# Kernel optimization log

Measured on AMD Instinct MI355X. Metric: run time of the kernel, lower is better.

Reference implementation:

```python
import jax, jax.numpy as jnp
import numpy as np

NUM_HEADS = 16

def setup_inputs() -> dict:
    key = jax.random.key(0)
    ks = jax.random.split(key, 8)
    B, S, X, D = 2, 2048, 1, 1024
    scale = 1.0 / np.sqrt(D)
    return {
        "query": jax.random.normal(ks[0], (B, S, X, D), jnp.float32),
        "key": jax.random.normal(ks[1], (B, S, X, D), jnp.float32),
        "value": jax.random.normal(ks[2], (B, S, X, D), jnp.float32),
        "Wq": jax.random.normal(ks[3], (D, D), jnp.float32) * scale,
        "bq": jnp.zeros((D,), jnp.float32),
        "Wk": jax.random.normal(ks[4], (D, D), jnp.float32) * scale,
        "bk": jnp.zeros((D,), jnp.float32),
        "Wv": jax.random.normal(ks[5], (D, D), jnp.float32) * scale,
        "bv": jnp.zeros((D,), jnp.float32),
        "Wo": jax.random.normal(ks[6], (D, D), jnp.float32) * scale,
        "bo": jnp.zeros((D,), jnp.float32),
    }

def _split_heads(x, B, H):
    # [B, S, X, D] -> [B, H, S*X, depth]
    D = x.shape[-1]
    return x.reshape(B, -1, H, D // H).transpose(0, 2, 1, 3)

def reference(query, key, value, Wq, bq, Wk, bk, Wv, bv, Wo, bo):
    B, S, X, D = query.shape
    H = NUM_HEADS
    q = _split_heads(query @ Wq + bq, B, H)   # [B,H,L,dh], L=S*X
    k = _split_heads(key @ Wk + bk, B, H)
    v = _split_heads(value @ Wv + bv, B, H)
    dh = k.shape[-1]
    logits = jnp.einsum("bhqd,bhkd->bhqk", q, k) / jnp.sqrt(jnp.float32(dh))
    attn = jax.nn.softmax(logits, axis=-1)
    out = jnp.einsum("bhqk,bhkd->bhqd", attn, v)   # [B,H,L,dh]
    out = out.transpose(0, 2, 1, 3).reshape(B, S, -1, D)  # [B,S,X,D]
    return out @ Wo + bo
```

## Files before the change

### kernel.cpp

```cpp
#include <hip/hip_runtime.h>
#include <cstdint>
#include <cstddef>

typedef __bf16 bf16x8 __attribute__((ext_vector_type(8)));
typedef float f32x4 __attribute__((ext_vector_type(4)));
typedef float f32x16 __attribute__((ext_vector_type(16)));
typedef unsigned short u16;
typedef unsigned int u32;

static constexpr int Bn = 2;
static constexpr int L  = 2048;
static constexpr int Dm = 1024;
static constexpr int H  = 16;
static constexpr int DH = 64;
static constexpr int M  = Bn * L;

#define SC 0.18033688f

__device__ __forceinline__ u16 f2bf(float f) {
    union { float f; u32 u; } v; v.f = f;
    u32 u = v.u + 0x7FFFu + ((v.u >> 16) & 1u);
    return (u16)(u >> 16);
}

__device__ __forceinline__ void gl2lds16(const void* g, void* l) {
    __builtin_amdgcn_global_load_lds(
        (const __attribute__((address_space(1))) u32*)(uintptr_t)g,
        (__attribute__((address_space(3))) u32*)(uintptr_t)l, 16, 0, 0);
}

__global__ __launch_bounds__(256) void convert_in(
    const float* __restrict__ q, const float* __restrict__ k, const float* __restrict__ v,
    u16* __restrict__ dst)
{
    const float* src = (blockIdx.y == 0) ? q : (blockIdx.y == 1) ? k : v;
    u16* d = dst + (size_t)blockIdx.y * M * Dm;
    const size_t t = (size_t)blockIdx.x * 256 + threadIdx.x;
    const float4* s4 = reinterpret_cast<const float4*>(src) + t * 2;
    float4 f0 = s4[0], f1 = s4[1];
    u16 o[8] = { f2bf(f0.x), f2bf(f0.y), f2bf(f0.z), f2bf(f0.w),
                 f2bf(f1.x), f2bf(f1.y), f2bf(f1.z), f2bf(f1.w) };
    reinterpret_cast<uint4*>(d)[t] = *reinterpret_cast<uint4*>(o);
}

__global__ __launch_bounds__(256) void convert_wt(
    const float* __restrict__ Wq, const float* __restrict__ Wk,
    const float* __restrict__ Wv, const float* __restrict__ Wo,
    u16* __restrict__ dst)
{
    __shared__ u16 Ts[64][72];
    const int z = blockIdx.z;
    const float* W = (z == 0) ? Wq : (z == 1) ? Wk : (z == 2) ? Wv : Wo;
    u16* o = dst + (size_t)z * Dm * Dm;
    const int n0 = blockIdx.x * 64, k0 = blockIdx.y * 64;
    const int tid = threadIdx.x;

    {
        const int kr = tid >> 2, nc = (tid & 3) * 16;
        const float* s = W + (size_t)(k0 + kr) * Dm + n0 + nc;
        const float4* s4 = reinterpret_cast<const float4*>(s);
        float4 a = s4[0], b = s4[1], c = s4[2], d = s4[3];
        u16 t[16] = { f2bf(a.x), f2bf(a.y), f2bf(a.z), f2bf(a.w),
                      f2bf(b.x), f2bf(b.y), f2bf(b.z), f2bf(b.w),
                      f2bf(c.x), f2bf(c.y), f2bf(c.z), f2bf(c.w),
                      f2bf(d.x), f2bf(d.y), f2bf(d.z), f2bf(d.w) };
        *reinterpret_cast<uint4*>(&Ts[kr][nc])     = reinterpret_cast<uint4*>(t)[0];
        *reinterpret_cast<uint4*>(&Ts[kr][nc + 8]) = reinterpret_cast<uint4*>(t)[1];
    }
    __syncthreads();
    {
        const int nr = tid >> 2, kc = (tid & 3) * 16;
        u16 w[16];
        #pragma unroll
        for (int j = 0; j < 16; ++j) w[j] = Ts[kc + j][nr];
        u16* dptr = o + (size_t)(n0 + nr) * Dm + k0 + kc;
        *reinterpret_cast<uint4*>(dptr)     = reinterpret_cast<uint4*>(w)[0];
        *reinterpret_cast<uint4*>(dptr + 8) = reinterpret_cast<uint4*>(w)[1];
    }
}

__global__ __launch_bounds__(256) void gemm_qkv(
    const u16* __restrict__ Abuf, const u16* __restrict__ Wtb,
    const float* __restrict__ bq, const float* __restrict__ bk, const float* __restrict__ bv,
    u16* __restrict__ Qh, u16* __restrict__ Kh, u16* __restrict__ Vh)
{
    __shared__ u16 As[128 * 32];
    __shared__ u16 Bs[128 * 32];
    const int tid = threadIdx.x;
    const int wave = tid >> 6, lane = tid & 63;
    const int quad = lane >> 4, l16 = lane & 15;
    const int wr = wave >> 1, wc = wave & 1;
    const int z = blockIdx.z;
    const u16* A  = Abuf + (size_t)z * M * Dm;
    const u16* Bt = Wtb  + (size_t)z * Dm * Dm;
    const float* bias = (z == 0) ? bq : (z == 1) ? bk : bv;
    u16* out = (z == 0) ? Qh : (z == 1) ? Kh : Vh;
    const int n0 = blockIdx.x * 128, m0 = blockIdx.y * 128;

    const int srow = lane >> 2;
    const int skc  = (lane & 3) * 8;

    f32x4 acc[4][4] = {};

    for (int k0 = 0; k0 < Dm; k0 += 32) {
        __syncthreads();
        #pragma unroll
        for (int i = 0; i < 2; ++i) {
            const int ra = i * 64 + wave * 16;
            gl2lds16(A  + (size_t)(m0 + ra + srow) * Dm + k0 + skc, &As[ra * 32]);
            gl2lds16(Bt + (size_t)(n0 + ra + srow) * Dm + k0 + skc, &Bs[ra * 32]);
        }
        __syncthreads();
        bf16x8 af[4], bf[4];
        #pragma unroll
        for (int t = 0; t < 4; ++t) {
            af[t] = *reinterpret_cast<const bf16x8*>(&As[(wr * 64 + t * 16 + l16) * 32 + quad * 8]);
            bf[t] = *reinterpret_cast<const bf16x8*>(&Bs[(wc * 64 + t * 16 + l16) * 32 + quad * 8]);
        }
        #pragma unroll
        for (int mt = 0; mt < 4; ++mt)
            #pragma unroll
            for (int nt = 0; nt < 4; ++nt)
                acc[mt][nt] = __builtin_amdgcn_mfma_f32_16x16x32_bf16(af[mt], bf[nt], acc[mt][nt], 0, 0, 0);
    }

    const float qscale = (z == 0) ? SC : 1.0f;
    #pragma unroll
    for (int nt = 0; nt < 4; ++nt) {
        const int n = n0 + wc * 64 + nt * 16 + l16;
        const float badd = bias[n];
        const int h = n >> 6, d = n & 63;
        #pragma unroll
        for (int mt = 0; mt < 4; ++mt) {
            #pragma unroll
            for (int r = 0; r < 4; ++r) {
                const int m = m0 + wr * 64 + mt * 16 + quad * 4 + r;
                const int bb = m >> 11, ll = m & 2047;
                out[(((size_t)(bb * H + h)) * L + ll) * DH + d] = f2bf((acc[mt][nt][r] + badd) * qscale);
            }
        }
    }
}

__global__ __launch_bounds__(256) void transpose_v(
    const u16* __restrict__ Vh, u16* __restrict__ Vth)
{
    __shared__ u16 Ts[64][72];
    const int kt = blockIdx.x, h = blockIdx.y, b = blockIdx.z;
    const int tid = threadIdx.x;
    const size_t hb = ((size_t)(b * H + h)) * L * DH;

    {
        const int kr = tid >> 2, dc = (tid & 3) * 16;
        const u16* s = Vh + hb + (size_t)(kt * 64 + kr) * DH + dc;
        *reinterpret_cast<uint4*>(&Ts[kr][dc])     = *reinterpret_cast<const uint4*>(s);
        *reinterpret_cast<uint4*>(&Ts[kr][dc + 8]) = *reinterpret_cast<const uint4*>(s + 8);
    }
    __syncthreads();
    {
        const int dr = tid >> 2, kc = (tid & 3) * 16;
        u16 w[16];
        #pragma unroll
        for (int j = 0; j < 16; ++j) w[j] = Ts[kc + j][dr];
        u16* dptr = Vth + hb + (size_t)dr * L + kt * 64 + kc;
        *reinterpret_cast<uint4*>(dptr)     = reinterpret_cast<uint4*>(w)[0];
        *reinterpret_cast<uint4*>(dptr + 8) = reinterpret_cast<uint4*>(w)[1];
    }
}

__global__ __launch_bounds__(256) void attn(
    const u16* __restrict__ Qh, const u16* __restrict__ Kh,
    const u16* __restrict__ Vth, u16* __restrict__ ctx)
{
    __shared__ u16 KV[2 * 64 * 64];
    __shared__ u16 Os[64 * 72];

    const int tid  = threadIdx.x;
    const int wave = tid >> 6, lane = tid & 63;
    const int l31  = lane & 31, hh = lane >> 5;
    const int qt = blockIdx.x, h = blockIdx.y, b = blockIdx.z;
    const size_t hb = ((size_t)(b * H + h)) * L * DH;

    const int q0 = qt * 128 + wave * 32;

    bf16x8 qf[4];
    {
        const u16* qp = Qh + hb + (size_t)(q0 + l31) * DH + hh * 8;
        #pragma unroll
        for (int c = 0; c < 4; ++c)
            qf[c] = *reinterpret_cast<const bf16x8*>(qp + c * 16);
    }

    const int r_off = lane >> 3;
    const int s_sl  = lane & 7;

    int vbK[2], vbV[2];
    #pragma unroll
    for (int t = 0; t < 2; ++t) {
        const int rr = t * 32 + l31;
        vbK[t] = rr * 128 + ((rr & 7) << 4);
        vbV[t] = 2 * 64 * 64 + rr * 128 + ((rr & 7) << 4);
    }
    const char* ldsb = (const char*)KV;

    float rsum = 0.f;
    f32x16 oacc[2] = {};

    for (int kt = 0; kt < L / 64; ++kt) {
        __syncthreads();
        #pragma unroll
        for (int i = 0; i < 2; ++i) {
            const int rr = wave * 16 + i * 8 + r_off;
            gl2lds16(Kh  + hb + (size_t)(kt * 64 + rr) * DH + ((s_sl ^ (rr & 7)) << 3),
                     (char*)KV + (wave * 16 + i * 8) * 128);
            gl2lds16(Vth + hb + (size_t)rr * L + kt * 64 + ((s_sl ^ (rr & 7)) << 3),
                     (char*)KV + 8192 + (wave * 16 + i * 8) * 128);
        }
        __syncthreads();

        f32x16 st[2] = {};
        #pragma unroll
        for (int t = 0; t < 2; ++t) {
            #pragma unroll
            for (int c = 0; c < 4; ++c) {
                bf16x8 kf = *reinterpret_cast<const bf16x8*>(ldsb + (vbK[t] ^ (((c << 1) | hh) << 4)));
                st[t] = __builtin_amdgcn_mfma_f32_32x32x16_bf16(kf, qf[c], st[t], 0, 0, 0);
            }
        }

        bf16x8 pfrag[4];
        #pragma unroll
        for (int t = 0; t < 2; ++t) {
            float p[16];
            #pragma unroll
            for (int r = 0; r < 16; ++r) {
                p[r] = __builtin_amdgcn_exp2f(st[t][r]);
                rsum += p[r];
            }
            #pragma unroll
            for (int g = 0; g < 2; ++g) {
                float* pg = p + g * 8;
                #pragma unroll
                for (int j = 0; j < 4; ++j) {
                    asm volatile("v_permlane32_swap_b32 %0, %1" : "+v"(pg[j]), "+v"(pg[j + 4]));
                }
                u16 pk[8];
                #pragma unroll
                for (int j = 0; j < 8; ++j) pk[j] = f2bf(pg[j]);
                pfrag[t * 2 + g] = *reinterpret_cast<bf16x8*>(pk);
            }
        }

        #pragma unroll
        for (int t = 0; t < 2; ++t) {
            #pragma unroll
            for (int c = 0; c < 4; ++c) {
                bf16x8 vf = *reinterpret_cast<const bf16x8*>(ldsb + (vbV[t] ^ (((c << 1) | hh) << 4)));
                oacc[t] = __builtin_amdgcn_mfma_f32_32x32x16_bf16(vf, pfrag[c], oacc[t], 0, 0, 0);
            }
        }
    }

    rsum += __shfl_xor(rsum, 32);
    const float inv = 1.0f / rsum;

    for (int pass = 0; pass < 2; ++pass) {
        __syncthreads();
        if ((wave >> 1) == pass) {
            const int qloc = (wave & 1) * 32 + l31;
            #pragma unroll
            for (int t = 0; t < 2; ++t)
                #pragma unroll
                for (int r = 0; r < 16; ++r) {
                    const int d = t * 32 + (r & 3) + ((r >> 2) << 3) + hh * 4;
                    Os[qloc * 72 + d] = f2bf(oacc[t][r] * inv);
                }
        }
        __syncthreads();
        {
            const int row = tid >> 2, cc = (tid & 3) * 16;
            u16* dst = ctx + ((size_t)(b * L + qt * 128 + pass * 64 + row)) * Dm + h * 64 + cc;
            *reinterpret_cast<uint4*>(dst)     = *reinterpret_cast<const uint4*>(&Os[row * 72 + cc]);
            *reinterpret_cast<uint4*>(dst + 8) = *reinterpret_cast<const uint4*>(&Os[row * 72 + cc + 8]);
        }
    }
}

__global__ __launch_bounds__(256) void gemm_out(
    const u16* __restrict__ A, const u16* __restrict__ Bt,
    const float* __restrict__ bias, float* __restrict__ out)
{
    __shared__ u16 As[128 * 32];
    __shared__ u16 Bs[64 * 32];
    const int tid = threadIdx.x;
    const int wave = tid >> 6, lane = tid & 63;
    const int quad = lane >> 4, l16 = lane & 15;
    const int n0 = blockIdx.x * 64, m0 = blockIdx.y * 128;

    const int srow = lane >> 2;
    const int skc  = (lane & 3) * 8;

    f32x4 acc[2][4] = {};

    for (int k0 = 0; k0 < Dm; k0 += 32) {
        __syncthreads();
        #pragma unroll
        for (int i = 0; i < 2; ++i) {
            const int ra = i * 64 + wave * 16;
            gl2lds16(A + (size_t)(m0 + ra + srow) * Dm + k0 + skc, &As[ra * 32]);
        }
        gl2lds16(Bt + (size_t)(n0 + wave * 16 + srow) * Dm + k0 + skc, &Bs[wave * 16 * 32]);
        __syncthreads();
        bf16x8 af[2], bf[4];
        #pragma unroll
        for (int t = 0; t < 2; ++t)
            af[t] = *reinterpret_cast<const bf16x8*>(&As[(wave * 32 + t * 16 + l16) * 32 + quad * 8]);
        #pragma unroll
        for (int t = 0; t < 4; ++t)
            bf[t] = *reinterpret_cast<const bf16x8*>(&Bs[(t * 16 + l16) * 32 + quad * 8]);
        #pragma unroll
        for (int mt = 0; mt < 2; ++mt)
            #pragma unroll
            for (int nt = 0; nt < 4; ++nt)
                acc[mt][nt] = __builtin_amdgcn_mfma_f32_16x16x32_bf16(af[mt], bf[nt], acc[mt][nt], 0, 0, 0);
    }

    #pragma unroll
    for (int nt = 0; nt < 4; ++nt) {
        const int n = n0 + nt * 16 + l16;
        const float badd = bias[n];
        #pragma unroll
        for (int mt = 0; mt < 2; ++mt) {
            #pragma unroll
            for (int r = 0; r < 4; ++r) {
                const int m = m0 + wave * 32 + mt * 16 + quad * 4 + r;
                out[(size_t)m * Dm + n] = acc[mt][nt][r] + badd;
            }
        }
    }
}

extern "C" void kernel_launch(void* const* d_in, const int* in_sizes, int n_in,
                              void* d_out, int out_size, void* d_ws, size_t ws_size,
                              hipStream_t stream) {
    const float* q  = (const float*)d_in[0];
    const float* k  = (const float*)d_in[1];
    const float* v  = (const float*)d_in[2];
    const float* Wq = (const float*)d_in[3];
    const float* bq = (const float*)d_in[4];
    const float* Wk = (const float*)d_in[5];
    const float* bk = (const float*)d_in[6];
    const float* Wv = (const float*)d_in[7];
    const float* bv = (const float*)d_in[8];
    const float* Wo = (const float*)d_in[9];
    const float* bo = (const float*)d_in[10];
    float* out = (float*)d_out;

    const size_t per = (size_t)Bn * H * L * DH;
    u16* Abuf = (u16*)d_ws;
    u16* Wt   = Abuf + 3 * (size_t)M * Dm;
    u16* Qh   = Wt + 4 * (size_t)Dm * Dm;
    u16* Kh   = Qh + per;
    u16* Vh   = Kh + per;
    u16* Vth  = Vh + per;
    u16* ctx  = Abuf;

    convert_in <<<dim3((M * Dm) / 8 / 256, 3), 256, 0, stream>>>(q, k, v, Abuf);
    convert_wt <<<dim3(Dm / 64, Dm / 64, 4), 256, 0, stream>>>(Wq, Wk, Wv, Wo, Wt);
    gemm_qkv   <<<dim3(Dm / 128, M / 128, 3), 256, 0, stream>>>(Abuf, Wt, bq, bk, bv, Qh, Kh, Vh);
    transpose_v<<<dim3(L / 64, H, Bn), 256, 0, stream>>>(Vh, Vth);
    attn       <<<dim3(L / 128, H, Bn), 256, 0, stream>>>(Qh, Kh, Vth, ctx);
    gemm_out   <<<dim3(Dm / 64, M / 128), 256, 0, stream>>>(ctx, Wt + 3 * (size_t)Dm * Dm, bo, out);
}
```

Baseline: 239.0 us.

## Double-buffer LDS tiles in GEMMs and attention, pack bf16 conversions

Each GEMM's K loop and the attention KV loop now use two LDS buffers. The next tile's global-to-LDS load is issued right after the barrier, so it overlaps the MFMA work on the current tile, and each iteration needs one barrier instead of two. Float-to-bf16 conversion now uses the packed hardware builtin when it is available, and the output stores in attention are written as packed 32-bit values. The cost is twice the LDS use in the GEMMs (attention now reserves 32 KB), which may lower occupancy. The attention output staging buffer reuses the first KV buffer, which depends on the barrier placed after the loop.

```diff
diff --git a/kernel.cpp b/kernel.cpp
--- a/kernel.cpp
+++ b/kernel.cpp
@@ -23,6 +23,17 @@
     return (u16)(u >> 16);
 }
 
+__device__ __forceinline__ u32 pk_bf16(float a, float b) {
+#if __has_builtin(__builtin_amdgcn_cvt_pk_bf16_f32)
+    typedef __bf16 bf16x2_t __attribute__((ext_vector_type(2)));
+    bf16x2_t t = __builtin_amdgcn_cvt_pk_bf16_f32(a, b);
+    u32 r; __builtin_memcpy(&r, &t, 4); return r;
+#else
+    return (u32)f2bf(a) | ((u32)f2bf(b) << 16);
+#endif
+}
+__device__ __forceinline__ u16 f2bf1(float f) { return (u16)(pk_bf16(f, f) & 0xffffu); }
+
 __device__ __forceinline__ void gl2lds16(const void* g, void* l) {
     __builtin_amdgcn_global_load_lds(
         (const __attribute__((address_space(1))) u32*)(uintptr_t)g,
@@ -38,8 +49,8 @@
     const size_t t = (size_t)blockIdx.x * 256 + threadIdx.x;
     const float4* s4 = reinterpret_cast<const float4*>(src) + t * 2;
     float4 f0 = s4[0], f1 = s4[1];
-    u16 o[8] = { f2bf(f0.x), f2bf(f0.y), f2bf(f0.z), f2bf(f0.w),
-                 f2bf(f1.x), f2bf(f1.y), f2bf(f1.z), f2bf(f1.w) };
+    u32 o[4] = { pk_bf16(f0.x, f0.y), pk_bf16(f0.z, f0.w),
+                 pk_bf16(f1.x, f1.y), pk_bf16(f1.z, f1.w) };
     reinterpret_cast<uint4*>(d)[t] = *reinterpret_cast<uint4*>(o);
 }
 
@@ -60,10 +71,8 @@
         const float* s = W + (size_t)(k0 + kr) * Dm + n0 + nc;
         const float4* s4 = reinterpret_cast<const float4*>(s);
         float4 a = s4[0], b = s4[1], c = s4[2], d = s4[3];
-        u16 t[16] = { f2bf(a.x), f2bf(a.y), f2bf(a.z), f2bf(a.w),
-                      f2bf(b.x), f2bf(b.y), f2bf(b.z), f2bf(b.w),
-                      f2bf(c.x), f2bf(c.y), f2bf(c.z), f2bf(c.w),
-                      f2bf(d.x), f2bf(d.y), f2bf(d.z), f2bf(d.w) };
+        u32 t[8] = { pk_bf16(a.x, a.y), pk_bf16(a.z, a.w), pk_bf16(b.x, b.y), pk_bf16(b.z, b.w),
+                     pk_bf16(c.x, c.y), pk_bf16(c.z, c.w), pk_bf16(d.x, d.y), pk_bf16(d.z, d.w) };
         *reinterpret_cast<uint4*>(&Ts[kr][nc])     = reinterpret_cast<uint4*>(t)[0];
         *reinterpret_cast<uint4*>(&Ts[kr][nc + 8]) = reinterpret_cast<uint4*>(t)[1];
     }
@@ -84,8 +93,8 @@
     const float* __restrict__ bq, const float* __restrict__ bk, const float* __restrict__ bv,
     u16* __restrict__ Qh, u16* __restrict__ Kh, u16* __restrict__ Vh)
 {
-    __shared__ u16 As[128 * 32];
-    __shared__ u16 Bs[128 * 32];
+    __shared__ u16 As[2][128 * 32];
+    __shared__ u16 Bs[2][128 * 32];
     const int tid = threadIdx.x;
     const int wave = tid >> 6, lane = tid & 63;
     const int quad = lane >> 4, l16 = lane & 15;
@@ -102,20 +111,25 @@
 
     f32x4 acc[4][4] = {};
 
-    for (int k0 = 0; k0 < Dm; k0 += 32) {
-        __syncthreads();
+    auto stage = [&](int k0, int bi) {
         #pragma unroll
         for (int i = 0; i < 2; ++i) {
             const int ra = i * 64 + wave * 16;
-            gl2lds16(A  + (size_t)(m0 + ra + srow) * Dm + k0 + skc, &As[ra * 32]);
-            gl2lds16(Bt + (size_t)(n0 + ra + srow) * Dm + k0 + skc, &Bs[ra * 32]);
-        }
+            gl2lds16(A  + (size_t)(m0 + ra + srow) * Dm + k0 + skc, &As[bi][ra * 32]);
+            gl2lds16(Bt + (size_t)(n0 + ra + srow) * Dm + k0 + skc, &Bs[bi][ra * 32]);
+        }
+    };
+
+    stage(0, 0);
+    for (int k0 = 0, it = 0; k0 < Dm; k0 += 32, ++it) {
+        const int cb = it & 1;
         __syncthreads();
+        if (k0 + 32 < Dm) stage(k0 + 32, cb ^ 1);
         bf16x8 af[4], bf[4];
         #pragma unroll
         for (int t = 0; t < 4; ++t) {
-            af[t] = *reinterpret_cast<const bf16x8*>(&As[(wr * 64 + t * 16 + l16) * 32 + quad * 8]);
-            bf[t] = *reinterpret_cast<const bf16x8*>(&Bs[(wc * 64 + t * 16 + l16) * 32 + quad * 8]);
+            af[t] = *reinterpret_cast<const bf16x8*>(&As[cb][(wr * 64 + t * 16 + l16) * 32 + quad * 8]);
+            bf[t] = *reinterpret_cast<const bf16x8*>(&Bs[cb][(wc * 64 + t * 16 + l16) * 32 + quad * 8]);
         }
         #pragma unroll
         for (int mt = 0; mt < 4; ++mt)
@@ -136,7 +150,7 @@
             for (int r = 0; r < 4; ++r) {
                 const int m = m0 + wr * 64 + mt * 16 + quad * 4 + r;
                 const int bb = m >> 11, ll = m & 2047;
-                out[(((size_t)(bb * H + h)) * L + ll) * DH + d] = f2bf((acc[mt][nt][r] + badd) * qscale);
+                out[(((size_t)(bb * H + h)) * L + ll) * DH + d] = f2bf1((acc[mt][nt][r] + badd) * qscale);
             }
         }
     }
@@ -172,15 +186,14 @@
     const u16* __restrict__ Qh, const u16* __restrict__ Kh,
     const u16* __restrict__ Vth, u16* __restrict__ ctx)
 {
-    __shared__ u16 KV[2 * 64 * 64];
-    __shared__ u16 Os[64 * 72];
+    __shared__ __align__(16) char smem[32768];
+    u16* Os = (u16*)smem;
 
     const int tid  = threadIdx.x;
     const int wave = tid >> 6, lane = tid & 63;
     const int l31  = lane & 31, hh = lane >> 5;
     const int qt = blockIdx.x, h = blockIdx.y, b = blockIdx.z;
     const size_t hb = ((size_t)(b * H + h)) * L * DH;
-
     const int q0 = qt * 128 + wave * 32;
 
     bf16x8 qf[4];
@@ -193,30 +206,36 @@
 
     const int r_off = lane >> 3;
     const int s_sl  = lane & 7;
+
+    auto stage = [&](int kt, int bi) {
+        char* base = smem + bi * 16384;
+        #pragma unroll
+        for (int i = 0; i < 2; ++i) {
+            const int rr = wave * 16 + i * 8 + r_off;
+            gl2lds16(Kh  + hb + (size_t)(kt * 64 + rr) * DH + ((s_sl ^ (rr & 7)) << 3),
+                     base + (wave * 16 + i * 8) * 128);
+            gl2lds16(Vth + hb + (size_t)rr * L + kt * 64 + ((s_sl ^ (rr & 7)) << 3),
+                     base + 8192 + (wave * 16 + i * 8) * 128);
+        }
+    };
 
     int vbK[2], vbV[2];
     #pragma unroll
     for (int t = 0; t < 2; ++t) {
         const int rr = t * 32 + l31;
         vbK[t] = rr * 128 + ((rr & 7) << 4);
-        vbV[t] = 2 * 64 * 64 + rr * 128 + ((rr & 7) << 4);
-    }
-    const char* ldsb = (const char*)KV;
+        vbV[t] = 8192 + rr * 128 + ((rr & 7) << 4);
+    }
 
     float rsum = 0.f;
     f32x16 oacc[2] = {};
 
+    stage(0, 0);
     for (int kt = 0; kt < L / 64; ++kt) {
+        const int cb = kt & 1;
         __syncthreads();
-        #pragma unroll
-        for (int i = 0; i < 2; ++i) {
-            const int rr = wave * 16 + i * 8 + r_off;
-            gl2lds16(Kh  + hb + (size_t)(kt * 64 + rr) * DH + ((s_sl ^ (rr & 7)) << 3),
-                     (char*)KV + (wave * 16 + i * 8) * 128);
-            gl2lds16(Vth + hb + (size_t)rr * L + kt * 64 + ((s_sl ^ (rr & 7)) << 3),
-                     (char*)KV + 8192 + (wave * 16 + i * 8) * 128);
-        }
-        __syncthreads();
+        if (kt + 1 < L / 64) stage(kt + 1, cb ^ 1);
+        const char* ldsb = smem + cb * 16384;
 
         f32x16 st[2] = {};
         #pragma unroll
@@ -233,21 +252,20 @@
         for (int t = 0; t < 2; ++t) {
             float p[16];
             #pragma unroll
-            for (int r = 0; r < 16; ++r) {
-                p[r] = __builtin_amdgcn_exp2f(st[t][r]);
-                rsum += p[r];
+            for (int rr = 0; rr < 16; ++rr) {
+                p[rr] = __builtin_amdgcn_exp2f(st[t][rr]);
+                rsum += p[rr];
             }
             #pragma unroll
             for (int g = 0; g < 2; ++g) {
                 float* pg = p + g * 8;
                 #pragma unroll
-                for (int j = 0; j < 4; ++j) {
+                for (int j = 0; j < 4; ++j)
                     asm volatile("v_permlane32_swap_b32 %0, %1" : "+v"(pg[j]), "+v"(pg[j + 4]));
-                }
-                u16 pk[8];
+                u32 pkv[4];
                 #pragma unroll
-                for (int j = 0; j < 8; ++j) pk[j] = f2bf(pg[j]);
-                pfrag[t * 2 + g] = *reinterpret_cast<bf16x8*>(pk);
+                for (int j = 0; j < 4; ++j) pkv[j] = pk_bf16(pg[2 * j], pg[2 * j + 1]);
+                pfrag[t * 2 + g] = *reinterpret_cast<bf16x8*>(pkv);
             }
         }
 
@@ -264,17 +282,22 @@
     rsum += __shfl_xor(rsum, 32);
     const float inv = 1.0f / rsum;
 
+    #pragma unroll
     for (int pass = 0; pass < 2; ++pass) {
         __syncthreads();
         if ((wave >> 1) == pass) {
             const int qloc = (wave & 1) * 32 + l31;
             #pragma unroll
-            for (int t = 0; t < 2; ++t)
+            for (int t = 0; t < 2; ++t) {
                 #pragma unroll
-                for (int r = 0; r < 16; ++r) {
-                    const int d = t * 32 + (r & 3) + ((r >> 2) << 3) + hh * 4;
-                    Os[qloc * 72 + d] = f2bf(oacc[t][r] * inv);
+                for (int rq = 0; rq < 4; ++rq) {
+                    const int d0 = t * 32 + rq * 8 + hh * 4;
+                    *reinterpret_cast<u32*>(&Os[qloc * 72 + d0]) =
+                        pk_bf16(oacc[t][rq * 4 + 0] * inv, oacc[t][rq * 4 + 1] * inv);
+                    *reinterpret_cast<u32*>(&Os[qloc * 72 + d0 + 2]) =
+                        pk_bf16(oacc[t][rq * 4 + 2] * inv, oacc[t][rq * 4 + 3] * inv);
                 }
+            }
         }
         __syncthreads();
         {
@@ -290,8 +313,8 @@
     const u16* __restrict__ A, const u16* __restrict__ Bt,
     const float* __restrict__ bias, float* __restrict__ out)
 {
-    __shared__ u16 As[128 * 32];
-    __shared__ u16 Bs[64 * 32];
+    __shared__ u16 As[2][128 * 32];
+    __shared__ u16 Bs[2][64 * 32];
     const int tid = threadIdx.x;
     const int wave = tid >> 6, lane = tid & 63;
     const int quad = lane >> 4, l16 = lane & 15;
@@ -302,22 +325,27 @@
 
     f32x4 acc[2][4] = {};
 
-    for (int k0 = 0; k0 < Dm; k0 += 32) {
-        __syncthreads();
+    auto stage = [&](int k0, int bi) {
         #pragma unroll
         for (int i = 0; i < 2; ++i) {
             const int ra = i * 64 + wave * 16;
-            gl2lds16(A + (size_t)(m0 + ra + srow) * Dm + k0 + skc, &As[ra * 32]);
-        }
-        gl2lds16(Bt + (size_t)(n0 + wave * 16 + srow) * Dm + k0 + skc, &Bs[wave * 16 * 32]);
+            gl2lds16(A + (size_t)(m0 + ra + srow) * Dm + k0 + skc, &As[bi][ra * 32]);
+        }
+        gl2lds16(Bt + (size_t)(n0 + wave * 16 + srow) * Dm + k0 + skc, &Bs[bi][wave * 16 * 32]);
+    };
+
+    stage(0, 0);
+    for (int k0 = 0, it = 0; k0 < Dm; k0 += 32, ++it) {
+        const int cb = it & 1;
         __syncthreads();
+        if (k0 + 32 < Dm) stage(k0 + 32, cb ^ 1);
         bf16x8 af[2], bf[4];
         #pragma unroll
         for (int t = 0; t < 2; ++t)
-            af[t] = *reinterpret_cast<const bf16x8*>(&As[(wave * 32 + t * 16 + l16) * 32 + quad * 8]);
+            af[t] = *reinterpret_cast<const bf16x8*>(&As[cb][(wave * 32 + t * 16 + l16) * 32 + quad * 8]);
         #pragma unroll
         for (int t = 0; t < 4; ++t)
-            bf[t] = *reinterpret_cast<const bf16x8*>(&Bs[(t * 16 + l16) * 32 + quad * 8]);
+            bf[t] = *reinterpret_cast<const bf16x8*>(&Bs[cb][(t * 16 + l16) * 32 + quad * 8]);
         #pragma unroll
         for (int mt = 0; mt < 2; ++mt)
             #pragma unroll
```

Result: no change. 237.8 us (-0.5%).
